# Optimization experiments

Hardware: AMD Instinct MI355X
Metric: run time of the kernel (lower is better)

Reference implementation:

```python
import jax, jax.numpy as jnp
import numpy as np

N = 100000
IN_DIM = 128
HID = 64
OUT = 4


def _gcn_conv(x, W, b, src, dst, deg_inv_sqrt):
    """PyG GCNConv: linear transform, then symmetric-normalized scatter-add.
    src/dst already include self-loops; deg_inv_sqrt precomputed over them."""
    h = x @ W                                   # [N, H]
    norm = deg_inv_sqrt[src] * deg_inv_sqrt[dst]  # [E+N]
    msg = h[src] * norm[:, None]                # gather + scale, [E+N, H]
    out = jax.ops.segment_sum(msg, dst, num_segments=N)  # scatter-add
    return out + b


def setup_inputs() -> dict:
    key = jax.random.key(0)
    ks = jax.random.split(key, 8)
    E = 1600000
    x = jax.random.normal(ks[0], (N, IN_DIM), dtype=jnp.float32)
    edge_index = jax.random.randint(ks[1], (2, E), 0, N, dtype=jnp.int32)
    # Glorot-ish init for weights
    W1 = jax.random.normal(ks[2], (IN_DIM, HID), dtype=jnp.float32) / np.sqrt(IN_DIM)
    b1 = jnp.zeros((HID,), dtype=jnp.float32)
    W2 = jax.random.normal(ks[3], (HID, HID), dtype=jnp.float32) / np.sqrt(HID)
    b2 = jnp.zeros((HID,), dtype=jnp.float32)
    Wfc = jax.random.normal(ks[4], (HID, OUT), dtype=jnp.float32) / np.sqrt(HID)
    bfc = jnp.zeros((OUT,), dtype=jnp.float32)
    return {"x": x, "edge_index": edge_index, "W1": W1, "b1": b1,
            "W2": W2, "b2": b2, "Wfc": Wfc, "bfc": bfc}


def reference(x, edge_index, W1, b1, W2, b2, Wfc, bfc):
    # Add self-loops (GCNConv default add_self_loops=True)
    loops = jnp.arange(N, dtype=edge_index.dtype)
    src = jnp.concatenate([edge_index[0], loops])
    dst = jnp.concatenate([edge_index[1], loops])
    # Symmetric normalization: deg computed at aggregation targets (dst)
    deg = jax.ops.segment_sum(jnp.ones_like(dst, dtype=x.dtype), dst,
                              num_segments=N)
    deg_inv_sqrt = jnp.where(deg > 0, jax.lax.rsqrt(deg), 0.0)

    h = _gcn_conv(x, W1, b1, src, dst, deg_inv_sqrt)
    h = jax.nn.relu(h)                 # dropout is identity in eval mode
    h = _gcn_conv(h, W2, b2, src, dst, deg_inv_sqrt)
    h = jax.nn.relu(h)
    return h @ Wfc + bfc               # [N, 4]
```

## Files before the change

kernel.cpp:

```cpp
#include <hip/hip_runtime.h>
#include <hip/hip_fp16.h>


#define BCAP 2560
#define BINB 512
#define CHUNK 3200
#define NBH  784
#define CAP  64
#define LCAP 32

typedef float v2f __attribute__((ext_vector_type(2)));
typedef _Float16 f16x8 __attribute__((ext_vector_type(8)));
typedef float f32x4 __attribute__((ext_vector_type(4)));

__global__ __launch_bounds__(256) void k_bin_gemm1(
        const int* __restrict__ src, const int* __restrict__ dst, int e,
        int* bcur, unsigned* __restrict__ binned,
        const float* __restrict__ X, const float* __restrict__ W1,
        __half* __restrict__ Hh, int n) {
    __shared__ union {
        struct {
            unsigned ec[CHUNK];
            unsigned short eb[CHUNK];
            int lh[NBH], lbase[NBH], lr[NBH];
        } b;
        struct {
            _Float16 As[128 * 136];
            _Float16 Bs[64 * 136];
        } g;
    } sm;

    int t = threadIdx.x;

    if ((int)blockIdx.x < BINB) {
        auto& B = sm.b;
        for (int i = t; i < NBH; i += 256) { B.lh[i] = 0; B.lr[i] = 0; }
        __syncthreads();
        int chunk = (e + BINB - 1) / BINB;
        int lo = blockIdx.x * chunk;
        int hi = min(e, lo + chunk);
        for (int i = lo + t; i < hi; i += 256) {
            int d = dst[i];
            int b = d >> 7;
            B.ec[i - lo] = ((unsigned)src[i] << 7) | (unsigned)(d & 127);
            B.eb[i - lo] = (unsigned short)b;
            atomicAdd(&B.lh[b], 1);
        }
        __syncthreads();
        for (int i = t; i < NBH; i += 256)
            B.lbase[i] = B.lh[i] ? atomicAdd(&bcur[i], B.lh[i]) : 0;
        __syncthreads();
        int cnt = hi - lo;
        for (int i = t; i < cnt; i += 256) {
            int b = B.eb[i];
            int r = B.lbase[b] + atomicAdd(&B.lr[b], 1);
            if (r < BCAP)
                binned[(size_t)b * BCAP + r] = B.ec[i];
        }
    } else {
        constexpr int K = 128, KP = 136;
        _Float16* As = sm.g.As;
        _Float16* Bs = sm.g.Bs;
        _Float16* H = (_Float16*)Hh;

        #pragma unroll
        for (int p = 0; p < 8; ++p) {
            int i = t + p * 256;
            int k = i >> 4, nn4 = (i & 15) << 2;
            float4 v = ((const float4*)W1)[i];
            Bs[(nn4 + 0) * KP + k] = (_Float16)v.x;
            Bs[(nn4 + 1) * KP + k] = (_Float16)v.y;
            Bs[(nn4 + 2) * KP + k] = (_Float16)v.z;
            Bs[(nn4 + 3) * KP + k] = (_Float16)v.w;
        }

        int row0 = ((int)blockIdx.x - BINB) * 128;
        #pragma unroll
        for (int p = 0; p < 8; ++p) {
            int gi  = t + p * 256;
            int row = gi >> 4, sg = gi & 15;
            int grow = row0 + row;
            float4 v0 = make_float4(0.f, 0.f, 0.f, 0.f), v1 = v0;
            if (grow < n) {
                v0 = *(const float4*)(X + (size_t)grow * K + sg * 8);
                v1 = *(const float4*)(X + (size_t)grow * K + sg * 8 + 4);
            }
            union { __half2 h[4]; float4 f; } u;
            u.h[0] = __floats2half2_rn(v0.x, v0.y);
            u.h[1] = __floats2half2_rn(v0.z, v0.w);
            u.h[2] = __floats2half2_rn(v1.x, v1.y);
            u.h[3] = __floats2half2_rn(v1.z, v1.w);
            *(float4*)(As + row * KP + sg * 8) = u.f;
        }
        __syncthreads();

        int wv   = t >> 6;
        int lane = t & 63;
        int m    = lane & 15;
        int quad = lane >> 4;
        int r0   = wv * 32;

        f32x4 acc[2][4] = {};
        #pragma unroll
        for (int kb = 0; kb < K / 32; ++kb) {
            f16x8 af0 = *(const f16x8*)(As + (r0 + m) * KP + quad * 8 + kb * 32);
            f16x8 af1 = *(const f16x8*)(As + (r0 + 16 + m) * KP + quad * 8 + kb * 32);
            #pragma unroll
            for (int nt = 0; nt < 4; ++nt) {
                f16x8 bf = *(const f16x8*)(Bs + (nt * 16 + m) * KP + quad * 8 + kb * 32);
                acc[0][nt] = __builtin_amdgcn_mfma_f32_16x16x32_f16(af0, bf, acc[0][nt], 0, 0, 0);
                acc[1][nt] = __builtin_amdgcn_mfma_f32_16x16x32_f16(af1, bf, acc[1][nt], 0, 0, 0);
            }
        }

        #pragma unroll
        for (int mt = 0; mt < 2; ++mt) {
            int gr[4];
            #pragma unroll
            for (int r = 0; r < 4; ++r)
                gr[r] = row0 + r0 + mt * 16 + quad * 4 + r;
            #pragma unroll
            for (int nt = 0; nt < 4; ++nt)
                #pragma unroll
                for (int r = 0; r < 4; ++r) {
                    if (gr[r] < n)
                        H[(size_t)gr[r] * 64 + nt * 16 + m] =
                            (_Float16)acc[mt][nt][r];
                    else if (gr[r] == n)
                        H[(size_t)n * 64 + nt * 16 + m] = (_Float16)0.f;
                }
        }
    }
}

__global__ __launch_bounds__(512) void k_bucket2(const unsigned* __restrict__ binned,
                                                 const int* __restrict__ bcur,
                                                 int n, int* __restrict__ cnt,
                                                 int* __restrict__ slots) {
    __shared__ int lists[128 * (LCAP + 1)];
    __shared__ int lcnt[128];
    int b = blockIdx.x, t = threadIdx.x;
    int node0 = b << 7;
    size_t ebase = (size_t)b * BCAP;
    int ecnt = min(bcur[b], BCAP);
    if (t < 128) lcnt[t] = 0;
    __syncthreads();
    for (int j = t; j < ecnt; j += 512) {
        unsigned ed = binned[ebase + j];
        int ld = ed & 127u;
        int s  = (int)(ed >> 7);
        int r  = atomicAdd(&lcnt[ld], 1);
        if (r < LCAP)
            lists[ld * (LCAP + 1) + r] = s;
        else if (r < CAP)
            slots[((size_t)(node0 + ld) << 6) + r] = s;
    }
    __syncthreads();
    if (t < 128 && node0 + t < n) cnt[node0 + t] = lcnt[t];
    for (int k = t; k < 128 * LCAP; k += 512) {
        int ld = k >> 5;
        int r  = k & (LCAP - 1);
        if (r < min(lcnt[ld], LCAP) && node0 + ld < n)
            slots[((size_t)(node0 + ld) << 6) + r] =
                lists[ld * (LCAP + 1) + r];
    }
}

__global__ __launch_bounds__(256) void k_gemm2(const __half* __restrict__ X,
                                               const float* __restrict__ W2,
                                               const int* __restrict__ cnt,
                                               __half* __restrict__ Hh, int n) {
    constexpr int K = 64, KP = 72;
    __shared__ _Float16 As[128 * KP];
    __shared__ _Float16 Bs[64 * KP];

    int t = threadIdx.x;
    _Float16* H = (_Float16*)Hh;

    #pragma unroll
    for (int p = 0; p < 4; ++p) {
        int i = t + p * 256;
        int k = i >> 4, nn4 = (i & 15) << 2;
        float4 v = ((const float4*)W2)[i];
        Bs[(nn4 + 0) * KP + k] = (_Float16)v.x;
        Bs[(nn4 + 1) * KP + k] = (_Float16)v.y;
        Bs[(nn4 + 2) * KP + k] = (_Float16)v.z;
        Bs[(nn4 + 3) * KP + k] = (_Float16)v.w;
    }

    int row0 = blockIdx.x * 128;
    const __half* Xh = X;
    #pragma unroll
    for (int p = 0; p < 4; ++p) {
        int gi  = t + p * 256;
        int row = gi >> 3, sg = gi & 7;
        int grow = row0 + row;
        float4 v = make_float4(0.f, 0.f, 0.f, 0.f);
        if (grow < n)
            v = *(const float4*)(Xh + (size_t)grow * K + sg * 8);
        *(float4*)(As + row * KP + sg * 8) = v;
    }
    __syncthreads();

    int wv   = t >> 6;
    int lane = t & 63;
    int m    = lane & 15;
    int quad = lane >> 4;
    int r0   = wv * 32;

    f32x4 acc[2][4] = {};
    #pragma unroll
    for (int kb = 0; kb < K / 32; ++kb) {
        f16x8 af0 = *(const f16x8*)(As + (r0 + m) * KP + quad * 8 + kb * 32);
        f16x8 af1 = *(const f16x8*)(As + (r0 + 16 + m) * KP + quad * 8 + kb * 32);
        #pragma unroll
        for (int nt = 0; nt < 4; ++nt) {
            f16x8 bf = *(const f16x8*)(Bs + (nt * 16 + m) * KP + quad * 8 + kb * 32);
            acc[0][nt] = __builtin_amdgcn_mfma_f32_16x16x32_f16(af0, bf, acc[0][nt], 0, 0, 0);
            acc[1][nt] = __builtin_amdgcn_mfma_f32_16x16x32_f16(af1, bf, acc[1][nt], 0, 0, 0);
        }
    }

    #pragma unroll
    for (int mt = 0; mt < 2; ++mt) {
        float dv[4]; int gr[4];
        #pragma unroll
        for (int r = 0; r < 4; ++r) {
            gr[r] = row0 + r0 + mt * 16 + quad * 4 + r;
            dv[r] = (gr[r] < n) ? rsqrtf((float)(cnt[gr[r]] + 1)) : 0.f;
        }
        #pragma unroll
        for (int nt = 0; nt < 4; ++nt)
            #pragma unroll
            for (int r = 0; r < 4; ++r) {
                if (gr[r] < n)
                    H[(size_t)gr[r] * 64 + nt * 16 + m] =
                        (_Float16)(acc[mt][nt][r] * dv[r]);
                else if (gr[r] == n)
                    H[(size_t)n * 64 + nt * 16 + m] = (_Float16)0.f;
            }
    }
}

__device__ inline void add_row(const __half* __restrict__ hp, int s, int c4,
                               v2f& lo, v2f& hi) {
    float2 raw = *(const float2*)(hp + (size_t)s * 64 + c4);
    const __half2* p = (const __half2*)&raw;
    float2 l = __half22float2(p[0]);
    float2 h = __half22float2(p[1]);
    lo += (v2f){ l.x, l.y };
    hi += (v2f){ h.x, h.y };
}

__device__ inline void fma_row(const __half* __restrict__ hp, int s, int c4,
                               float w, v2f& lo, v2f& hi) {
    float2 raw = *(const float2*)(hp + (size_t)s * 64 + c4);
    const __half2* p = (const __half2*)&raw;
    float2 l = __half22float2(p[0]);
    float2 h = __half22float2(p[1]);
    lo += w * (v2f){ l.x, l.y };
    hi += w * (v2f){ h.x, h.y };
}

template<bool FUSE, bool SCALE>
__global__ __launch_bounds__(256) void k_gather(const __half* __restrict__ hp,
                                                const int* __restrict__ slots,
                                                const int* __restrict__ cnt,
                                                const float* __restrict__ bias,
                                                void* __restrict__ outb,
                                                const float* __restrict__ Wfc,
                                                const float* __restrict__ bfc,
                                                int n) {
    int lane = threadIdx.x & 63;
    int wid  = (blockIdx.x * blockDim.x + threadIdx.x) >> 6;
    if (wid >= n) return;
    int d    = wid;
    int esub = lane >> 4;
    int c4   = (lane & 15) * 4;

    size_t start = (size_t)d << 6;
    int num = cnt[d];
    int lim = min(num, CAP);
    int idx = (lane < lim) ? slots[start + lane] : 0;
    float dsv = 0.f;
    if constexpr (SCALE)
        dsv = rsqrtf((float)(cnt[idx] + 1));
    float dd = rsqrtf((float)(num + 1));

    v2f aL[4] = {}, aH[4] = {};
    if (esub == 0) {
        if constexpr (SCALE) fma_row(hp, d, c4, dd, aL[0], aH[0]);
        else                 add_row(hp, d, c4, aL[0], aH[0]);
    }

    int j = 0;
    for (; j + 16 <= lim; j += 16) {
        int s0 = __shfl(idx, j + esub);
        int s1 = __shfl(idx, j + 4 + esub);
        int s2 = __shfl(idx, j + 8 + esub);
        int s3 = __shfl(idx, j + 12 + esub);
        if constexpr (SCALE) {
            float w0 = __shfl(dsv, j + esub);
            float w1 = __shfl(dsv, j + 4 + esub);
            float w2 = __shfl(dsv, j + 8 + esub);
            float w3 = __shfl(dsv, j + 12 + esub);
            fma_row(hp, s0, c4, w0, aL[0], aH[0]);
            fma_row(hp, s1, c4, w1, aL[1], aH[1]);
            fma_row(hp, s2, c4, w2, aL[2], aH[2]);
            fma_row(hp, s3, c4, w3, aL[3], aH[3]);
        } else {
            add_row(hp, s0, c4, aL[0], aH[0]);
            add_row(hp, s1, c4, aL[1], aH[1]);
            add_row(hp, s2, c4, aL[2], aH[2]);
            add_row(hp, s3, c4, aL[3], aH[3]);
        }
    }
    for (; j < lim; j += 4) {
        int jj = j + esub;
        int sr = __shfl(idx, jj);
        int s  = (jj < lim) ? sr : n;
        if constexpr (SCALE) {
            float w = __shfl(dsv, jj);
            fma_row(hp, s, c4, w, aL[0], aH[0]);
        } else {
            add_row(hp, s, c4, aL[0], aH[0]);
        }
    }
    v2f sL = (aL[0] + aL[1]) + (aL[2] + aL[3]);
    v2f sH = (aH[0] + aH[1]) + (aH[2] + aH[3]);
    float4 a0 = make_float4(sL.x, sL.y, sH.x, sH.y);
    #pragma unroll
    for (int o = 16; o <= 32; o <<= 1) {
        a0.x += __shfl_xor(a0.x, o);
        a0.y += __shfl_xor(a0.y, o);
        a0.z += __shfl_xor(a0.z, o);
        a0.w += __shfl_xor(a0.w, o);
    }
    float4 bb = *(const float4*)(bias + c4);
    float4 o;
    o.x = fmaxf(bb.x + dd * a0.x, 0.f);
    o.y = fmaxf(bb.y + dd * a0.y, 0.f);
    o.z = fmaxf(bb.z + dd * a0.z, 0.f);
    o.w = fmaxf(bb.w + dd * a0.w, 0.f);
    if (!FUSE) {
        if (esub == 0) {
            union { __half2 h[2]; float2 f; } u;
            u.h[0] = __floats2half2_rn(o.x, o.y);
            u.h[1] = __floats2half2_rn(o.z, o.w);
            *(float2*)((__half*)outb + (size_t)d * 64 + c4) = u.f;
        }
    } else {
        const float4* W4 = (const float4*)Wfc;
        float4 w0 = W4[c4 + 0], w1 = W4[c4 + 1], w2 = W4[c4 + 2], w3 = W4[c4 + 3];
        float4 p;
        p.x = o.x * w0.x + o.y * w1.x + o.z * w2.x + o.w * w3.x;
        p.y = o.x * w0.y + o.y * w1.y + o.z * w2.y + o.w * w3.y;
        p.z = o.x * w0.z + o.y * w1.z + o.z * w2.z + o.w * w3.z;
        p.w = o.x * w0.w + o.y * w1.w + o.z * w2.w + o.w * w3.w;
        #pragma unroll
        for (int q = 1; q <= 8; q <<= 1) {
            p.x += __shfl_xor(p.x, q);
            p.y += __shfl_xor(p.y, q);
            p.z += __shfl_xor(p.z, q);
            p.w += __shfl_xor(p.w, q);
        }
        if (lane == 0) {
            float4 bf = *(const float4*)bfc;
            float4 r = make_float4(p.x + bf.x, p.y + bf.y, p.z + bf.z, p.w + bf.w);
            ((float4*)outb)[d] = r;
        }
    }
}

static inline size_t align256(size_t x) { return (x + 255) & ~(size_t)255; }

extern "C" void kernel_launch(void* const* d_in, const int* in_sizes, int n_in,
                              void* d_out, int out_size, void* d_ws, size_t ws_size,
                              hipStream_t stream) {
    const float* x   = (const float*)d_in[0];
    const int*   ei  = (const int*)d_in[1];
    const float* W1  = (const float*)d_in[2];
    const float* b1  = (const float*)d_in[3];
    const float* W2  = (const float*)d_in[4];
    const float* b2  = (const float*)d_in[5];
    const float* Wfc = (const float*)d_in[6];
    const float* bfc = (const float*)d_in[7];
    float* out = (float*)d_out;

    int n = in_sizes[0] / 128;
    int e = in_sizes[1] / 2;
    const int* src = ei;
    const int* dst = ei + e;

    char* ws = (char*)d_ws;
    size_t p = 0;
    int*      cnt    = (int*)     (ws + p); p = align256(p + (size_t)n * 4);
    int*      bcur   = (int*)     (ws + p); p = align256(p + NBH * 4);
    unsigned* binned = (unsigned*)(ws + p); p = align256(p + (size_t)NBH * BCAP * 4);
    int*      slots  = (int*)     (ws + p); p = align256(p + (size_t)n * CAP * 4);
    __half*   hbuf   = (__half*)  (ws + p); p = align256(p + (size_t)(n + 1) * 64 * 2);
    __half*   a1h    = (__half*)  (ws + p);

    int gb  = (n + 127) / 128;
    int nbk = (n + 127) / 128;

    hipMemsetAsync(bcur, 0, NBH * sizeof(int), stream);
    k_bin_gemm1<<<BINB + gb, 256, 0, stream>>>(src, dst, e, bcur, binned,
                                               x, W1, hbuf, n);
    k_bucket2<<<nbk, 512, 0, stream>>>(binned, bcur, n, cnt, slots);

    k_gather<false, true><<<(n * 64 + 255) / 256, 256, 0, stream>>>(
        hbuf, slots, cnt, b1, a1h, nullptr, nullptr, n);

    k_gemm2<<<gb, 256, 0, stream>>>(a1h, W2, cnt, hbuf, n);
    k_gather<true, false><<<(n * 64 + 255) / 256, 256, 0, stream>>>(
        hbuf, slots, cnt, b2, out, Wfc, bfc, n);
}
```

Before: 250.1 us.

## Split gather1 in halves and overlap second half with gemm2 of first half

The first aggregation now runs over the first H nodes on its own. A combined kernel then runs the remaining gather1 nodes in some blocks while other blocks run gemm2 on the already finished first half, and a final kernel does gemm2 on the tail. gemm2 is refactored into 64-row tiles, and a separate output buffer is added so gemm2 no longer overwrites the buffer gather1 is reading. The aim is to hide gemm2 inside the memory-bound gather, at the cost of an extra launch, an extra workspace buffer, and a hardcoded split point tied to N.

```diff
diff --git a/kernel.cpp b/kernel.cpp
--- a/kernel.cpp
+++ b/kernel.cpp
@@ -166,15 +166,12 @@
     }
 }
 
-__global__ __launch_bounds__(256) void k_gemm2(const __half* __restrict__ X,
-                                               const float* __restrict__ W2,
-                                               const int* __restrict__ cnt,
-                                               __half* __restrict__ Hh, int n) {
+__device__ inline void gemm2_64(const __half* __restrict__ X,
+                                const float* __restrict__ W2,
+                                const int* __restrict__ cnt,
+                                __half* __restrict__ Hh, int n, int row0,
+                                int t, _Float16* As, _Float16* Bs) {
     constexpr int K = 64, KP = 72;
-    __shared__ _Float16 As[128 * KP];
-    __shared__ _Float16 Bs[64 * KP];
-
-    int t = threadIdx.x;
     _Float16* H = (_Float16*)Hh;
 
     #pragma unroll
@@ -188,10 +185,9 @@
         Bs[(nn4 + 3) * KP + k] = (_Float16)v.w;
     }
 
-    int row0 = blockIdx.x * 128;
-    const __half* Xh = X;
-    #pragma unroll
-    for (int p = 0; p < 4; ++p) {
+    const _Float16* Xh = (const _Float16*)X;
+    #pragma unroll
+    for (int p = 0; p < 2; ++p) {
         int gi  = t + p * 256;
         int row = gi >> 3, sg = gi & 7;
         int grow = row0 + row;
@@ -206,40 +202,45 @@
     int lane = t & 63;
     int m    = lane & 15;
     int quad = lane >> 4;
-    int r0   = wv * 32;
-
-    f32x4 acc[2][4] = {};
+    int r0   = wv * 16;
+
+    f32x4 acc[4] = {};
     #pragma unroll
     for (int kb = 0; kb < K / 32; ++kb) {
-        f16x8 af0 = *(const f16x8*)(As + (r0 + m) * KP + quad * 8 + kb * 32);
-        f16x8 af1 = *(const f16x8*)(As + (r0 + 16 + m) * KP + quad * 8 + kb * 32);
+        f16x8 af = *(const f16x8*)(As + (r0 + m) * KP + quad * 8 + kb * 32);
         #pragma unroll
         for (int nt = 0; nt < 4; ++nt) {
             f16x8 bf = *(const f16x8*)(Bs + (nt * 16 + m) * KP + quad * 8 + kb * 32);
-            acc[0][nt] = __builtin_amdgcn_mfma_f32_16x16x32_f16(af0, bf, acc[0][nt], 0, 0, 0);
-            acc[1][nt] = __builtin_amdgcn_mfma_f32_16x16x32_f16(af1, bf, acc[1][nt], 0, 0, 0);
-        }
-    }
-
-    #pragma unroll
-    for (int mt = 0; mt < 2; ++mt) {
-        float dv[4]; int gr[4];
+            acc[nt] = __builtin_amdgcn_mfma_f32_16x16x32_f16(af, bf, acc[nt], 0, 0, 0);
+        }
+    }
+
+    float dv[4]; int gr[4];
+    #pragma unroll
+    for (int r = 0; r < 4; ++r) {
+        gr[r] = row0 + r0 + quad * 4 + r;
+        dv[r] = (gr[r] < n) ? rsqrtf((float)(cnt[gr[r]] + 1)) : 0.f;
+    }
+    #pragma unroll
+    for (int nt = 0; nt < 4; ++nt)
         #pragma unroll
         for (int r = 0; r < 4; ++r) {
-            gr[r] = row0 + r0 + mt * 16 + quad * 4 + r;
-            dv[r] = (gr[r] < n) ? rsqrtf((float)(cnt[gr[r]] + 1)) : 0.f;
-        }
-        #pragma unroll
-        for (int nt = 0; nt < 4; ++nt)
-            #pragma unroll
-            for (int r = 0; r < 4; ++r) {
-                if (gr[r] < n)
-                    H[(size_t)gr[r] * 64 + nt * 16 + m] =
-                        (_Float16)(acc[mt][nt][r] * dv[r]);
-                else if (gr[r] == n)
-                    H[(size_t)n * 64 + nt * 16 + m] = (_Float16)0.f;
-            }
-    }
+            if (gr[r] < n)
+                H[(size_t)gr[r] * 64 + nt * 16 + m] =
+                    (_Float16)(acc[nt][r] * dv[r]);
+            else if (gr[r] == n)
+                H[(size_t)n * 64 + nt * 16 + m] = (_Float16)0.f;
+        }
+}
+
+__global__ __launch_bounds__(256) void k_gemm2(const __half* __restrict__ X,
+                                               const float* __restrict__ W2,
+                                               const int* __restrict__ cnt,
+                                               __half* __restrict__ Hh,
+                                               int rbase, int n) {
+    __shared__ _Float16 As[64 * 72];
+    __shared__ _Float16 Bs[64 * 72];
+    gemm2_64(X, W2, cnt, Hh, n, rbase + (int)blockIdx.x * 64, threadIdx.x, As, Bs);
 }
 
 __device__ inline void add_row(const __half* __restrict__ hp, int s, int c4,
@@ -262,15 +263,110 @@
     hi += w * (v2f){ h.x, h.y };
 }
 
-template<bool FUSE, bool SCALE>
-__global__ __launch_bounds__(256) void k_gather(const __half* __restrict__ hp,
-                                                const int* __restrict__ slots,
-                                                const int* __restrict__ cnt,
-                                                const float* __restrict__ bias,
-                                                void* __restrict__ outb,
-                                                const float* __restrict__ Wfc,
-                                                const float* __restrict__ bfc,
-                                                int n) {
+__device__ inline void gather1_node(const __half* __restrict__ hp,
+                                    const int* __restrict__ slots,
+                                    const int* __restrict__ cnt,
+                                    const float* __restrict__ bias,
+                                    __half* __restrict__ outh,
+                                    int d, int lane, int n) {
+    int esub = lane >> 4;
+    int c4   = (lane & 15) * 4;
+    size_t start = (size_t)d << 6;
+    int num = cnt[d];
+    int lim = min(num, CAP);
+    int idx = (lane < lim) ? slots[start + lane] : 0;
+    float dsv = rsqrtf((float)(cnt[idx] + 1));
+    float dd  = rsqrtf((float)(num + 1));
+
+    v2f aL[4] = {}, aH[4] = {};
+    if (esub == 0)
+        fma_row(hp, d, c4, dd, aL[0], aH[0]);
+
+    int j = 0;
+    for (; j + 16 <= lim; j += 16) {
+        int s0 = __shfl(idx, j + esub);
+        int s1 = __shfl(idx, j + 4 + esub);
+        int s2 = __shfl(idx, j + 8 + esub);
+        int s3 = __shfl(idx, j + 12 + esub);
+        float w0 = __shfl(dsv, j + esub);
+        float w1 = __shfl(dsv, j + 4 + esub);
+        float w2 = __shfl(dsv, j + 8 + esub);
+        float w3 = __shfl(dsv, j + 12 + esub);
+        fma_row(hp, s0, c4, w0, aL[0], aH[0]);
+        fma_row(hp, s1, c4, w1, aL[1], aH[1]);
+        fma_row(hp, s2, c4, w2, aL[2], aH[2]);
+        fma_row(hp, s3, c4, w3, aL[3], aH[3]);
+    }
+    for (; j < lim; j += 4) {
+        int jj = j + esub;
+        int sr = __shfl(idx, jj);
+        int s  = (jj < lim) ? sr : n;
+        float w = __shfl(dsv, jj);
+        fma_row(hp, s, c4, w, aL[0], aH[0]);
+    }
+    v2f sL = (aL[0] + aL[1]) + (aL[2] + aL[3]);
+    v2f sH = (aH[0] + aH[1]) + (aH[2] + aH[3]);
+    float4 a0 = make_float4(sL.x, sL.y, sH.x, sH.y);
+    #pragma unroll
+    for (int o = 16; o <= 32; o <<= 1) {
+        a0.x += __shfl_xor(a0.x, o);
+        a0.y += __shfl_xor(a0.y, o);
+        a0.z += __shfl_xor(a0.z, o);
+        a0.w += __shfl_xor(a0.w, o);
+    }
+    float4 bb = *(const float4*)(bias + c4);
+    float4 o;
+    o.x = fmaxf(bb.x + dd * a0.x, 0.f);
+    o.y = fmaxf(bb.y + dd * a0.y, 0.f);
+    o.z = fmaxf(bb.z + dd * a0.z, 0.f);
+    o.w = fmaxf(bb.w + dd * a0.w, 0.f);
+    if (esub == 0) {
+        union { __half2 h[2]; float2 f; } u;
+        u.h[0] = __floats2half2_rn(o.x, o.y);
+        u.h[1] = __floats2half2_rn(o.z, o.w);
+        *(float2*)((__half*)outh + (size_t)d * 64 + c4) = u.f;
+    }
+}
+
+__global__ __launch_bounds__(256) void k_gather1(const __half* __restrict__ hp,
+                                                 const int* __restrict__ slots,
+                                                 const int* __restrict__ cnt,
+                                                 const float* __restrict__ bias,
+                                                 __half* __restrict__ outh,
+                                                 int wid0, int wlim, int n) {
+    int lane = threadIdx.x & 63;
+    int wid  = wid0 + ((blockIdx.x * blockDim.x + threadIdx.x) >> 6);
+    if (wid >= wlim) return;
+    gather1_node(hp, slots, cnt, bias, outh, wid, lane, n);
+}
+
+__global__ __launch_bounds__(256) void k_gth1_gemm2(
+        const __half* __restrict__ hp, const int* __restrict__ slots,
+        const int* __restrict__ cnt, const float* __restrict__ b1,
+        __half* __restrict__ a1h, const float* __restrict__ W2,
+        __half* __restrict__ h2, int GB1, int H, int n) {
+    __shared__ _Float16 As[64 * 72];
+    __shared__ _Float16 Bs[64 * 72];
+    int t = threadIdx.x;
+    if ((int)blockIdx.x < GB1) {
+        int lane = t & 63;
+        int wid  = H + (((int)blockIdx.x * 256 + t) >> 6);
+        if (wid < n)
+            gather1_node(hp, slots, cnt, b1, a1h, wid, lane, n);
+    } else {
+        int row0 = ((int)blockIdx.x - GB1) * 64;
+        gemm2_64((const __half*)a1h, W2, cnt, h2, n, row0, t, As, Bs);
+    }
+}
+
+__global__ __launch_bounds__(256) void k_gather_fc(const __half* __restrict__ hp,
+                                                   const int* __restrict__ slots,
+                                                   const int* __restrict__ cnt,
+                                                   const float* __restrict__ bias,
+                                                   float* __restrict__ outb,
+                                                   const float* __restrict__ Wfc,
+                                                   const float* __restrict__ bfc,
+                                                   int n) {
     int lane = threadIdx.x & 63;
     int wid  = (blockIdx.x * blockDim.x + threadIdx.x) >> 6;
     if (wid >= n) return;
@@ -282,16 +378,11 @@
     int num = cnt[d];
     int lim = min(num, CAP);
     int idx = (lane < lim) ? slots[start + lane] : 0;
-    float dsv = 0.f;
-    if constexpr (SCALE)
-        dsv = rsqrtf((float)(cnt[idx] + 1));
     float dd = rsqrtf((float)(num + 1));
 
     v2f aL[4] = {}, aH[4] = {};
-    if (esub == 0) {
-        if constexpr (SCALE) fma_row(hp, d, c4, dd, aL[0], aH[0]);
-        else                 add_row(hp, d, c4, aL[0], aH[0]);
-    }
+    if (esub == 0)
+        add_row(hp, d, c4, aL[0], aH[0]);
 
     int j = 0;
     for (; j + 16 <= lim; j += 16) {
@@ -299,32 +390,16 @@
         int s1 = __shfl(idx, j + 4 + esub);
         int s2 = __shfl(idx, j + 8 + esub);
         int s3 = __shfl(idx, j + 12 + esub);
-        if constexpr (SCALE) {
-            float w0 = __shfl(dsv, j + esub);
-            float w1 = __shfl(dsv, j + 4 + esub);
-            float w2 = __shfl(dsv, j + 8 + esub);
-            float w3 = __shfl(dsv, j + 12 + esub);
-            fma_row(hp, s0, c4, w0, aL[0], aH[0]);
-            fma_row(hp, s1, c4, w1, aL[1], aH[1]);
-            fma_row(hp, s2, c4, w2, aL[2], aH[2]);
-            fma_row(hp, s3, c4, w3, aL[3], aH[3]);
-        } else {
-            add_row(hp, s0, c4, aL[0], aH[0]);
-            add_row(hp, s1, c4, aL[1], aH[1]);
-            add_row(hp, s2, c4, aL[2], aH[2]);
-            add_row(hp, s3, c4, aL[3], aH[3]);
-        }
+        add_row(hp, s0, c4, aL[0], aH[0]);
+        add_row(hp, s1, c4, aL[1], aH[1]);
+        add_row(hp, s2, c4, aL[2], aH[2]);
+        add_row(hp, s3, c4, aL[3], aH[3]);
     }
     for (; j < lim; j += 4) {
         int jj = j + esub;
         int sr = __shfl(idx, jj);
         int s  = (jj < lim) ? sr : n;
-        if constexpr (SCALE) {
-            float w = __shfl(dsv, jj);
-            fma_row(hp, s, c4, w, aL[0], aH[0]);
-        } else {
-            add_row(hp, s, c4, aL[0], aH[0]);
-        }
+        add_row(hp, s, c4, aL[0], aH[0]);
     }
     v2f sL = (aL[0] + aL[1]) + (aL[2] + aL[3]);
     v2f sH = (aH[0] + aH[1]) + (aH[2] + aH[3]);
@@ -342,33 +417,25 @@
     o.y = fmaxf(bb.y + dd * a0.y, 0.f);
     o.z = fmaxf(bb.z + dd * a0.z, 0.f);
     o.w = fmaxf(bb.w + dd * a0.w, 0.f);
-    if (!FUSE) {
-        if (esub == 0) {
-            union { __half2 h[2]; float2 f; } u;
-            u.h[0] = __floats2half2_rn(o.x, o.y);
-            u.h[1] = __floats2half2_rn(o.z, o.w);
-            *(float2*)((__half*)outb + (size_t)d * 64 + c4) = u.f;
-        }
-    } else {
-        const float4* W4 = (const float4*)Wfc;
-        float4 w0 = W4[c4 + 0], w1 = W4[c4 + 1], w2 = W4[c4 + 2], w3 = W4[c4 + 3];
-        float4 p;
-        p.x = o.x * w0.x + o.y * w1.x + o.z * w2.x + o.w * w3.x;
-        p.y = o.x * w0.y + o.y * w1.y + o.z * w2.y + o.w * w3.y;
-        p.z = o.x * w0.z + o.y * w1.z + o.z * w2.z + o.w * w3.z;
-        p.w = o.x * w0.w + o.y * w1.w + o.z * w2.w + o.w * w3.w;
-        #pragma unroll
-        for (int q = 1; q <= 8; q <<= 1) {
-            p.x += __shfl_xor(p.x, q);
-            p.y += __shfl_xor(p.y, q);
-            p.z += __shfl_xor(p.z, q);
-            p.w += __shfl_xor(p.w, q);
-        }
-        if (lane == 0) {
-            float4 bf = *(const float4*)bfc;
-            float4 r = make_float4(p.x + bf.x, p.y + bf.y, p.z + bf.z, p.w + bf.w);
-            ((float4*)outb)[d] = r;
-        }
+
+    const float4* W4 = (const float4*)Wfc;
+    float4 w0 = W4[c4 + 0], w1 = W4[c4 + 1], w2 = W4[c4 + 2], w3 = W4[c4 + 3];
+    float4 p;
+    p.x = o.x * w0.x + o.y * w1.x + o.z * w2.x + o.w * w3.x;
+    p.y = o.x * w0.y + o.y * w1.y + o.z * w2.y + o.w * w3.y;
+    p.z = o.x * w0.z + o.y * w1.z + o.z * w2.z + o.w * w3.z;
+    p.w = o.x * w0.w + o.y * w1.w + o.z * w2.w + o.w * w3.w;
+    #pragma unroll
+    for (int q = 1; q <= 8; q <<= 1) {
+        p.x += __shfl_xor(p.x, q);
+        p.y += __shfl_xor(p.y, q);
+        p.z += __shfl_xor(p.z, q);
+        p.w += __shfl_xor(p.w, q);
+    }
+    if (lane == 0) {
+        float4 bf = *(const float4*)bfc;
+        float4 r = make_float4(p.x + bf.x, p.y + bf.y, p.z + bf.z, p.w + bf.w);
+        ((float4*)outb)[d] = r;
     }
 }
 
@@ -399,20 +466,28 @@
     unsigned* binned = (unsigned*)(ws + p); p = align256(p + (size_t)NBH * BCAP * 4);
     int*      slots  = (int*)     (ws + p); p = align256(p + (size_t)n * CAP * 4);
     __half*   hbuf   = (__half*)  (ws + p); p = align256(p + (size_t)(n + 1) * 64 * 2);
-    __half*   a1h    = (__half*)  (ws + p);
+    __half*   a1h    = (__half*)  (ws + p); p = align256(p + (size_t)(n + 1) * 64 * 2);
+    __half*   hbuf2  = (__half*)  (ws + p);
 
     int gb  = (n + 127) / 128;
     int nbk = (n + 127) / 128;
+
+    int H    = 50048;
+    int g1a  = H / 4;
+    int GB1  = (n - H) / 4;
+    int gt2a = H / 64;
+    int gt2b = (n - H + 64) / 64;
 
     hipMemsetAsync(bcur, 0, NBH * sizeof(int), stream);
     k_bin_gemm1<<<BINB + gb, 256, 0, stream>>>(src, dst, e, bcur, binned,
                                                x, W1, hbuf, n);
     k_bucket2<<<nbk, 512, 0, stream>>>(binned, bcur, n, cnt, slots);
 
-    k_gather<false, true><<<(n * 64 + 255) / 256, 256, 0, stream>>>(
-        hbuf, slots, cnt, b1, a1h, nullptr, nullptr, n);
-
-    k_gemm2<<<gb, 256, 0, stream>>>(a1h, W2, cnt, hbuf, n);
-    k_gather<true, false><<<(n * 64 + 255) / 256, 256, 0, stream>>>(
-        hbuf, slots, cnt, b2, out, Wfc, bfc, n);
-}
+    k_gather1<<<g1a, 256, 0, stream>>>(hbuf, slots, cnt, b1, a1h, 0, H, n);
+    k_gth1_gemm2<<<GB1 + gt2a, 256, 0, stream>>>(hbuf, slots, cnt, b1, a1h,
+                                                 W2, hbuf2, GB1, H, n);
+    k_gemm2<<<gt2b, 256, 0, stream>>>(a1h, W2, cnt, hbuf2, H, n);
+
+    k_gather_fc<<<(n * 64 + 255) / 256, 256, 0, stream>>>(
+        hbuf2, slots, cnt, b2, out, Wfc, bfc, n);
+}
```

After: 254.9 us. Within noise of the previous version (+1.9%).
